# Kernel tuning notes

Hardware: AMD Instinct MI355X
Metric: run time of the kernel (lower is better)

The kernel has to match this reference:

```python
import jax, jax.numpy as jnp
import numpy as np

# Static configuration (mirrors init_kwargs)
F_REAL = 64
F_CAT = 32
OUT = 32
HID = [64, 64, 32]
IDX_REAL_MISS = np.arange(16)   # indices into the real-feature subset
IDX_CAT_MISS = np.arange(8)     # indices into the cat-feature subset
N_CAT_MISS = len(IDX_CAT_MISS)
B = 8192


def wn(v, g):
    """PyTorch weight_norm: w = g * v / ||v|| with norm over input dim (last axis).
    v: [F, out, in], g: [F, out] -> w: [F, out, in]"""
    return g[..., None] * v / jnp.linalg.norm(v, axis=-1, keepdims=True)


def setup_inputs() -> dict:
    key = jax.random.key(0)
    ks = jax.random.split(key, 16)
    s = 0.3
    values = jax.random.normal(ks[0], (B, 96), dtype=jnp.float32)
    miss = (jax.random.uniform(ks[1], (B, 96)) < 0.1).astype(jnp.float32)
    tabular = jnp.stack([values, miss], axis=1)  # [B, 2, 96]
    # Per-feature weight-normed MLP params, stacked over F_REAL features.
    inp = {
        "tabular": tabular,
        "v0": jax.random.normal(ks[2], (F_REAL, HID[0], 1)) * s,
        "g0": jnp.ones((F_REAL, HID[0])),
        "b0": jax.random.normal(ks[3], (F_REAL, HID[0])) * 0.01,
        "v1": jax.random.normal(ks[4], (F_REAL, HID[1], HID[0])) * s,
        "g1": jnp.ones((F_REAL, HID[1])),
        "b1": jax.random.normal(ks[5], (F_REAL, HID[1])) * 0.01,
        "v2": jax.random.normal(ks[6], (F_REAL, HID[2], HID[1])) * s,
        "g2": jnp.ones((F_REAL, HID[2])),
        "b2": jax.random.normal(ks[7], (F_REAL, HID[2])) * 0.01,
        "v3": jax.random.normal(ks[8], (F_REAL, OUT, HID[2])) * s,
        "g3": jnp.ones((F_REAL, OUT)),
        "cat_linear": jax.random.normal(ks[9], (F_CAT, OUT)) * s,
        "missing_emb": jax.random.normal(ks[10], (len(IDX_REAL_MISS) + N_CAT_MISS, OUT)) * s,
        "bias": jnp.zeros((1, OUT)),
    }
    return inp


def reference(tabular, v0, g0, b0, v1, g1, b1, v2, g2, b2, v3, g3,
              cat_linear, missing_emb, bias):
    # Eval mode: nn.Dropout / nn.Dropout1d are identity.
    values, is_missing = tabular[:, 0], tabular[:, 1]
    val_real, miss_real = values[:, :F_REAL], is_missing[:, :F_REAL]
    val_cat, miss_cat = values[:, F_REAL:F_REAL + F_CAT], is_missing[:, F_REAL:F_REAL + F_CAT]

    # Batched tiny MLPs over all real features at once.
    w0 = wn(v0, g0)[:, :, 0]                  # [F, H0] (scalar input)
    h = jax.nn.relu(val_real[:, :, None] * w0[None] + b0[None])        # [B,F,H0]
    h = jax.nn.relu(jnp.einsum('bfi,foi->bfo', h, wn(v1, g1)) + b1[None])  # [B,F,H1]
    h = jax.nn.relu(jnp.einsum('bfi,foi->bfo', h, wn(v2, g2)) + b2[None])  # [B,F,H2]
    feat_real = jnp.einsum('bfi,foi->bfo', h, wn(v3, g3))               # [B,F,OUT]

    feat_cat = cat_linear[None] * val_cat[:, :, None]                   # [B,Fc,OUT]

    feat_real = feat_real * (1.0 - miss_real[:, :, None])
    feat_cat = feat_cat * (1.0 - miss_cat[:, :, None])

    # Scatter-fill missing embeddings (add is exact since masked entries are zero)
    feat_real = feat_real.at[:, IDX_REAL_MISS, :].add(
        missing_emb[N_CAT_MISS:][None] * miss_real[:, IDX_REAL_MISS, None])
    feat_cat = feat_cat.at[:, IDX_CAT_MISS, :].add(
        missing_emb[:N_CAT_MISS][None] * miss_cat[:, IDX_CAT_MISS, None])

    features = jnp.concatenate([feat_real, feat_cat], axis=1)           # [B,96,OUT]
    logits = jnp.sum(features, axis=1) + bias                           # [B,OUT]
    return (logits, features)
```

## Files before the change

kernel.cpp:

```cpp
#include <hip/hip_runtime.h>
#include <math.h>

typedef _Float16 f16;
typedef _Float16 f16x8 __attribute__((ext_vector_type(8)));
typedef float f32x4 __attribute__((ext_vector_type(4)));

#define NB 8192
#define LOGN (NB * 32)

#define OFF_W0   0
#define OFF_SC1  16384
#define OFF_SC2  32768
#define OFF_SC3  40960
#define OFF_B1   49152
#define OFF_B2   573440
#define OFF_B3   835584
#define OFF_PART 966656
#define WS_NEED  (OFF_PART + 8ull * LOGN * 4ull)

__global__ __launch_bounds__(256)
void prep_norm(const float* __restrict__ v0, const float* __restrict__ g0,
               const float* __restrict__ v1, const float* __restrict__ g1,
               const float* __restrict__ v2, const float* __restrict__ g2,
               const float* __restrict__ v3, const float* __restrict__ g3,
               float* __restrict__ ws) {
    int t = blockIdx.x * blockDim.x + threadIdx.x;
    if (t < 4096) {
        float v = v0[t];
        ws[OFF_W0 / 4 + t] = g0[t] * (v >= 0.f ? 1.f : -1.f);
    } else if (t < 8192) {
        int r = t - 4096;
        const float* vp = v1 + (size_t)r * 64;
        float ss = 0.f;
        #pragma unroll
        for (int i = 0; i < 16; ++i) {
            float4 x = *(const float4*)(vp + i * 4);
            ss += x.x * x.x + x.y * x.y + x.z * x.z + x.w * x.w;
        }
        ws[OFF_SC1 / 4 + r] = g1[r] * __frsqrt_rn(ss);
    } else if (t < 10240) {
        int r = t - 8192;
        const float* vp = v2 + (size_t)r * 64;
        float ss = 0.f;
        #pragma unroll
        for (int i = 0; i < 16; ++i) {
            float4 x = *(const float4*)(vp + i * 4);
            ss += x.x * x.x + x.y * x.y + x.z * x.z + x.w * x.w;
        }
        ws[OFF_SC2 / 4 + r] = g2[r] * __frsqrt_rn(ss);
    } else if (t < 12288) {
        int r = t - 10240;
        const float* vp = v3 + (size_t)r * 32;
        float ss = 0.f;
        #pragma unroll
        for (int i = 0; i < 8; ++i) {
            float4 x = *(const float4*)(vp + i * 4);
            ss += x.x * x.x + x.y * x.y + x.z * x.z + x.w * x.w;
        }
        ws[OFF_SC3 / 4 + r] = g3[r] * __frsqrt_rn(ss);
    }
}

__global__ __launch_bounds__(256)
void prep_frag(const float* __restrict__ v1, const float* __restrict__ v2,
               const float* __restrict__ v3, const float* __restrict__ ws,
               f16* __restrict__ b1f, f16* __restrict__ b2f, f16* __restrict__ b3f) {
    int t = blockIdx.x * blockDim.x + threadIdx.x;
    if (t < 262144) {
        int i = t & 7, lane = (t >> 3) & 63, nt = (t >> 9) & 3, ks = (t >> 11) & 1, f = t >> 12;
        int k = ks * 32 + ((lane >> 4) << 3) + i;
        int n = nt * 16 + (lane & 15);
        int r = f * 64 + n;
        b1f[t] = (f16)(v1[(size_t)r * 64 + k] * ws[OFF_SC1 / 4 + r]);
    } else if (t < 393216) {
        int t2 = t - 262144;
        int i = t2 & 7, lane = (t2 >> 3) & 63, nt = (t2 >> 9) & 1, ks = (t2 >> 10) & 1, f = t2 >> 11;
        int k = ks * 32 + ((lane >> 4) << 3) + i;
        int n = nt * 16 + (lane & 15);
        int r = f * 32 + n;
        b2f[t2] = (f16)(v2[(size_t)r * 64 + k] * ws[OFF_SC2 / 4 + r]);
    } else {
        int t3 = t - 393216;
        int i = t3 & 7, lane = (t3 >> 3) & 63, nt = (t3 >> 9) & 1, f = t3 >> 10;
        int k = ((lane >> 4) << 3) + i;
        int n = nt * 16 + (lane & 15);
        int r = f * 32 + n;
        b3f[t3] = (f16)(v3[(size_t)r * 32 + k] * ws[OFF_SC3 / 4 + r]);
    }
}

__global__ __launch_bounds__(256, 2)
void nam_real_mfma(const float* __restrict__ tab, const float* __restrict__ w0,
                   const f16* __restrict__ b1f, const f16* __restrict__ b2f,
                   const f16* __restrict__ b3f,
                   const float* __restrict__ b0, const float* __restrict__ b1,
                   const float* __restrict__ b2, const float* __restrict__ memb,
                   float* __restrict__ feat, float* __restrict__ part) {
    __shared__ char lds[4][8192];
    __shared__ float tv[128][8];
    __shared__ float tm[128][8];
    const int wave = threadIdx.x >> 6, lane = threadIdx.x & 63;
    const int lq = lane >> 4, lr = lane & 15;
    const int rowbase = blockIdx.x * 128 + wave * 32;
    const int f0 = blockIdx.y * 8;
    char* h1b = lds[wave];
    char* h2b = lds[wave] + 4096;

    #pragma unroll
    for (int it = 0; it < 8; ++it) {
        int g = it * 256 + threadIdx.x;
        int row = g >> 4, w = g & 15;
        int col = (w < 8) ? (f0 + w) : (96 + f0 + (w - 8));
        float x = tab[(size_t)(blockIdx.x * 128 + row) * 192 + col];
        if (w < 8) tv[row][w] = x; else tm[row][w - 8] = x;
    }
    __syncthreads();

    float lacc[2][2][4];
    #pragma unroll
    for (int mt = 0; mt < 2; ++mt)
        #pragma unroll
        for (int nt = 0; nt < 2; ++nt)
            #pragma unroll
            for (int j = 0; j < 4; ++j) lacc[mt][nt][j] = 0.f;

    #pragma unroll 1
    for (int fi = 0; fi < 8; ++fi) {
        const int f = f0 + fi;

        f16x8 B1[2][4], B2[2][2], B3[2];
        {
            const f16* p1 = b1f + f * 4096 + lane * 8;
            #pragma unroll
            for (int ks = 0; ks < 2; ++ks)
                #pragma unroll
                for (int nt = 0; nt < 4; ++nt)
                    B1[ks][nt] = *(const f16x8*)(p1 + ks * 2048 + nt * 512);
            const f16* p2 = b2f + f * 2048 + lane * 8;
            #pragma unroll
            for (int ks = 0; ks < 2; ++ks)
                #pragma unroll
                for (int nt = 0; nt < 2; ++nt)
                    B2[ks][nt] = *(const f16x8*)(p2 + ks * 1024 + nt * 512);
            const f16* p3 = b3f + f * 1024 + lane * 8;
            #pragma unroll
            for (int nt = 0; nt < 2; ++nt)
                B3[nt] = *(const f16x8*)(p3 + nt * 512);
        }

        float b1v[4], b2v[2];
        #pragma unroll
        for (int nt = 0; nt < 4; ++nt) b1v[nt] = b1[f * 64 + nt * 16 + lr];
        #pragma unroll
        for (int nt = 0; nt < 2; ++nt) b2v[nt] = b2[f * 32 + nt * 16 + lr];
        float vmt[2];
        #pragma unroll
        for (int mt = 0; mt < 2; ++mt)
            vmt[mt] = tv[wave * 32 + mt * 16 + lr][fi];
        float ms[2][4];
        #pragma unroll
        for (int mt = 0; mt < 2; ++mt)
            #pragma unroll
            for (int j = 0; j < 4; ++j)
                ms[mt][j] = tm[wave * 32 + mt * 16 + lq * 4 + j][fi];

        f16x8 A0[2][2];
        #pragma unroll
        for (int ks = 0; ks < 2; ++ks) {
            float w0v[8], b0v[8];
            *(float4*)&w0v[0] = *(const float4*)(w0 + f * 64 + ks * 32 + lq * 8);
            *(float4*)&w0v[4] = *(const float4*)(w0 + f * 64 + ks * 32 + lq * 8 + 4);
            *(float4*)&b0v[0] = *(const float4*)(b0 + f * 64 + ks * 32 + lq * 8);
            *(float4*)&b0v[4] = *(const float4*)(b0 + f * 64 + ks * 32 + lq * 8 + 4);
            #pragma unroll
            for (int mt = 0; mt < 2; ++mt)
                #pragma unroll
                for (int i = 0; i < 8; ++i)
                    A0[mt][ks][i] = (f16)fmaxf(fmaf(vmt[mt], w0v[i], b0v[i]), 0.f);
        }

        f32x4 acc1[2][4];
        #pragma unroll
        for (int mt = 0; mt < 2; ++mt)
            #pragma unroll
            for (int nt = 0; nt < 4; ++nt) acc1[mt][nt] = (f32x4){0.f, 0.f, 0.f, 0.f};
        #pragma unroll
        for (int ks = 0; ks < 2; ++ks)
            #pragma unroll
            for (int nt = 0; nt < 4; ++nt)
                #pragma unroll
                for (int mt = 0; mt < 2; ++mt)
                    acc1[mt][nt] = __builtin_amdgcn_mfma_f32_16x16x32_f16(A0[mt][ks], B1[ks][nt], acc1[mt][nt], 0, 0, 0);
        #pragma unroll
        for (int mt = 0; mt < 2; ++mt)
            #pragma unroll
            for (int nt = 0; nt < 4; ++nt) {
                int n = nt * 16 + lr;
                int colb = ((n >> 3) << 4) + ((n & 7) << 1);
                #pragma unroll
                for (int j = 0; j < 4; ++j) {
                    int row = mt * 16 + lq * 4 + j;
                    int byte = ((row << 7) + colb) ^ ((row & 7) << 4);
                    *(f16*)(h1b + byte) = (f16)fmaxf(acc1[mt][nt][j] + b1v[nt], 0.f);
                }
            }

        f16x8 A1[2][2];
        #pragma unroll
        for (int mt = 0; mt < 2; ++mt)
            #pragma unroll
            for (int ks = 0; ks < 2; ++ks) {
                int row = mt * 16 + lr;
                int byte = ((row << 7) + ((ks * 4 + lq) << 4)) ^ ((row & 7) << 4);
                A1[mt][ks] = *(const f16x8*)(h1b + byte);
            }
        f32x4 acc2[2][2];
        #pragma unroll
        for (int mt = 0; mt < 2; ++mt)
            #pragma unroll
            for (int nt = 0; nt < 2; ++nt) acc2[mt][nt] = (f32x4){0.f, 0.f, 0.f, 0.f};
        #pragma unroll
        for (int ks = 0; ks < 2; ++ks)
            #pragma unroll
            for (int nt = 0; nt < 2; ++nt)
                #pragma unroll
                for (int mt = 0; mt < 2; ++mt)
                    acc2[mt][nt] = __builtin_amdgcn_mfma_f32_16x16x32_f16(A1[mt][ks], B2[ks][nt], acc2[mt][nt], 0, 0, 0);
        #pragma unroll
        for (int mt = 0; mt < 2; ++mt)
            #pragma unroll
            for (int nt = 0; nt < 2; ++nt) {
                int n = nt * 16 + lr;
                int colb = ((n >> 3) << 4) + ((n & 7) << 1);
                #pragma unroll
                for (int j = 0; j < 4; ++j) {
                    int row = mt * 16 + lq * 4 + j;
                    int byte = ((row << 7) + colb) ^ ((row & 7) << 4);
                    *(f16*)(h2b + byte) = (f16)fmaxf(acc2[mt][nt][j] + b2v[nt], 0.f);
                }
            }

        f16x8 A2[2];
        #pragma unroll
        for (int mt = 0; mt < 2; ++mt) {
            int row = mt * 16 + lr;
            int byte = ((row << 7) + (lq << 4)) ^ ((row & 7) << 4);
            A2[mt] = *(const f16x8*)(h2b + byte);
        }
        f32x4 acc3[2][2];
        #pragma unroll
        for (int mt = 0; mt < 2; ++mt)
            #pragma unroll
            for (int nt = 0; nt < 2; ++nt) acc3[mt][nt] = (f32x4){0.f, 0.f, 0.f, 0.f};
        #pragma unroll
        for (int nt = 0; nt < 2; ++nt)
            #pragma unroll
            for (int mt = 0; mt < 2; ++mt)
                acc3[mt][nt] = __builtin_amdgcn_mfma_f32_16x16x32_f16(A2[mt], B3[nt], acc3[mt][nt], 0, 0, 0);

        float e[2] = {0.f, 0.f};
        const bool hasemb = (f < 16);
        if (hasemb) {
            #pragma unroll
            for (int nt = 0; nt < 2; ++nt) e[nt] = memb[(8 + f) * 32 + nt * 16 + lr];
        }
        #pragma unroll
        for (int mt = 0; mt < 2; ++mt)
            #pragma unroll
            for (int nt = 0; nt < 2; ++nt) {
                int o = nt * 16 + lr;
                #pragma unroll
                for (int j = 0; j < 4; ++j) {
                    int row = rowbase + mt * 16 + lq * 4 + j;
                    float keep = 1.f - ms[mt][j];
                    float v = acc3[mt][nt][j] * keep;
                    if (hasemb) v = fmaf(e[nt], ms[mt][j], v);
                    feat[(size_t)row * 3072 + f * 32 + o] = v;
                    lacc[mt][nt][j] += v;
                }
            }
    }

    if (part) {
        float* pp = part + (size_t)blockIdx.y * LOGN;
        #pragma unroll
        for (int mt = 0; mt < 2; ++mt)
            #pragma unroll
            for (int nt = 0; nt < 2; ++nt)
                #pragma unroll
                for (int j = 0; j < 4; ++j) {
                    int row = rowbase + mt * 16 + lq * 4 + j;
                    pp[row * 32 + nt * 16 + lr] = lacc[mt][nt][j];
                }
    }
}

__global__ __launch_bounds__(256)
void nam_cat_reduce(const float* __restrict__ tab, const float* __restrict__ cat_linear,
                    const float* __restrict__ memb, const float* __restrict__ bias,
                    const float* __restrict__ part, float* __restrict__ feat,
                    float* __restrict__ logits) {
    int t = blockIdx.x * blockDim.x + threadIdx.x;
    int o = t & 31;
    int b = t >> 5;
    const float* tb = tab + (size_t)b * 192;
    float s = bias[o];
    if (part) {
        #pragma unroll
        for (int g = 0; g < 8; ++g) s += part[g * LOGN + t];
    }
    #pragma unroll
    for (int fc = 0; fc < 32; ++fc) {
        float val = tb[64 + fc];
        float miss = tb[160 + fc];
        float r = cat_linear[fc * 32 + o] * val * (1.f - miss);
        if (fc < 8) r = fmaf(memb[fc * 32 + o], miss, r);
        feat[(size_t)b * 3072 + (64 + fc) * 32 + o] = r;
        s += r;
    }
    if (part) logits[t] = s;
}

__global__ __launch_bounds__(256)
void nam_logits(const float* __restrict__ feat, const float* __restrict__ bias,
                float* __restrict__ logits) {
    int t = blockIdx.x * blockDim.x + threadIdx.x;
    int o = t & 31;
    int b = t >> 5;
    float s = bias[o];
    const float* fp = feat + (size_t)b * 3072 + o;
    #pragma unroll 8
    for (int f = 0; f < 96; ++f) s += fp[f * 32];
    logits[t] = s;
}

extern "C" void kernel_launch(void* const* d_in, const int* in_sizes, int n_in,
                              void* d_out, int out_size, void* d_ws, size_t ws_size,
                              hipStream_t stream) {
    const float* tab        = (const float*)d_in[0];
    const float* v0         = (const float*)d_in[1];
    const float* g0         = (const float*)d_in[2];
    const float* b0         = (const float*)d_in[3];
    const float* v1         = (const float*)d_in[4];
    const float* g1         = (const float*)d_in[5];
    const float* b1         = (const float*)d_in[6];
    const float* v2         = (const float*)d_in[7];
    const float* g2         = (const float*)d_in[8];
    const float* b2         = (const float*)d_in[9];
    const float* v3         = (const float*)d_in[10];
    const float* g3         = (const float*)d_in[11];
    const float* cat_linear = (const float*)d_in[12];
    const float* memb       = (const float*)d_in[13];
    const float* bias       = (const float*)d_in[14];

    float* out    = (float*)d_out;
    float* logits = out;
    float* feat   = out + LOGN;

    float* ws   = (float*)d_ws;
    float* w0   = (float*)((char*)d_ws + OFF_W0);
    f16*   b1f  = (f16*)((char*)d_ws + OFF_B1);
    f16*   b2f  = (f16*)((char*)d_ws + OFF_B2);
    f16*   b3f  = (f16*)((char*)d_ws + OFF_B3);
    float* part = (float*)((char*)d_ws + OFF_PART);
    const bool use_part = ws_size >= WS_NEED;
    float* partp = use_part ? part : nullptr;

    prep_norm<<<48, 256, 0, stream>>>(v0, g0, v1, g1, v2, g2, v3, g3, ws);
    prep_frag<<<1792, 256, 0, stream>>>(v1, v2, v3, ws, b1f, b2f, b3f);

    dim3 gr(64, 8);
    nam_real_mfma<<<gr, 256, 0, stream>>>(tab, w0, b1f, b2f, b3f, b0, b1, b2, memb, feat, partp);

    nam_cat_reduce<<<LOGN / 256, 256, 0, stream>>>(tab, cat_linear, memb, bias, partp, feat, logits);

    if (!use_part)
        nam_logits<<<LOGN / 256, 256, 0, stream>>>(feat, bias, logits);
}
```

Baseline: 48.00 us.

## Run cat kernel first and accumulate real-feature logits via atomics, transposed MFMA stores

The categorical kernel now runs before the MLP kernel, writing bias plus categorical contributions directly into logits. The real-feature kernel then atomically adds its per-block partial sums into logits, which removes the partial-sum workspace and the separate reduction pass. The layer-3 MFMA operands are swapped so each lane holds four contiguous output columns, allowing float4 feature stores instead of scalar stores. In exchange, the final logits depend on eight atomic adds per element, so summation order is no longer deterministic.

Result: slower. 72.84 us (+51.7%).

```diff
diff --git a/kernel.cpp b/kernel.cpp
--- a/kernel.cpp
+++ b/kernel.cpp
@@ -15,8 +15,6 @@
 #define OFF_B1   49152
 #define OFF_B2   573440
 #define OFF_B3   835584
-#define OFF_PART 966656
-#define WS_NEED  (OFF_PART + 8ull * LOGN * 4ull)
 
 __global__ __launch_bounds__(256)
 void prep_norm(const float* __restrict__ v0, const float* __restrict__ g0,
@@ -89,13 +87,49 @@
     }
 }
 
+__global__ __launch_bounds__(256)
+void nam_cat_base(const float* __restrict__ tab, const float* __restrict__ cat_linear,
+                  const float* __restrict__ memb, const float* __restrict__ bias,
+                  float* __restrict__ feat, float* __restrict__ logits) {
+    __shared__ float cl[1024];
+    __shared__ float mb[256];
+    __shared__ float bs[32];
+    for (int i = threadIdx.x; i < 1024; i += 256) cl[i] = cat_linear[i];
+    if (threadIdx.x < 256) mb[threadIdx.x] = memb[threadIdx.x];
+    if (threadIdx.x < 32) bs[threadIdx.x] = bias[threadIdx.x];
+    __syncthreads();
+
+    int t = blockIdx.x * blockDim.x + threadIdx.x;
+    int o = t & 31;
+    int b = t >> 5;
+    const float4* tb4 = (const float4*)(tab + (size_t)b * 192);
+    float* fb = feat + (size_t)b * 3072 + 64 * 32 + o;
+    float s = bs[o];
+    #pragma unroll
+    for (int q = 0; q < 8; ++q) {
+        float4 v4 = tb4[16 + q];
+        float4 m4 = tb4[40 + q];
+        float vv[4] = {v4.x, v4.y, v4.z, v4.w};
+        float mm[4] = {m4.x, m4.y, m4.z, m4.w};
+        #pragma unroll
+        for (int e = 0; e < 4; ++e) {
+            int fc = q * 4 + e;
+            float r = cl[fc * 32 + o] * vv[e] * (1.f - mm[e]);
+            if (fc < 8) r = fmaf(mb[fc * 32 + o], mm[e], r);
+            fb[fc * 32] = r;
+            s += r;
+        }
+    }
+    logits[t] = s;
+}
+
 __global__ __launch_bounds__(256, 2)
 void nam_real_mfma(const float* __restrict__ tab, const float* __restrict__ w0,
                    const f16* __restrict__ b1f, const f16* __restrict__ b2f,
                    const f16* __restrict__ b3f,
                    const float* __restrict__ b0, const float* __restrict__ b1,
                    const float* __restrict__ b2, const float* __restrict__ memb,
-                   float* __restrict__ feat, float* __restrict__ part) {
+                   float* __restrict__ feat, float* __restrict__ logits) {
     __shared__ char lds[4][8192];
     __shared__ float tv[128][8];
     __shared__ float tm[128][8];
@@ -153,16 +187,12 @@
         for (int nt = 0; nt < 4; ++nt) b1v[nt] = b1[f * 64 + nt * 16 + lr];
         #pragma unroll
         for (int nt = 0; nt < 2; ++nt) b2v[nt] = b2[f * 32 + nt * 16 + lr];
-        float vmt[2];
-        #pragma unroll
-        for (int mt = 0; mt < 2; ++mt)
+        float vmt[2], msr[2];
+        #pragma unroll
+        for (int mt = 0; mt < 2; ++mt) {
             vmt[mt] = tv[wave * 32 + mt * 16 + lr][fi];
-        float ms[2][4];
-        #pragma unroll
-        for (int mt = 0; mt < 2; ++mt)
-            #pragma unroll
-            for (int j = 0; j < 4; ++j)
-                ms[mt][j] = tm[wave * 32 + mt * 16 + lq * 4 + j][fi];
+            msr[mt] = tm[wave * 32 + mt * 16 + lr][fi];
+        }
 
         f16x8 A0[2][2];
         #pragma unroll
@@ -247,91 +277,62 @@
             int byte = ((row << 7) + (lq << 4)) ^ ((row & 7) << 4);
             A2[mt] = *(const f16x8*)(h2b + byte);
         }
-        f32x4 acc3[2][2];
-        #pragma unroll
-        for (int mt = 0; mt < 2; ++mt)
-            #pragma unroll
-            for (int nt = 0; nt < 2; ++nt) acc3[mt][nt] = (f32x4){0.f, 0.f, 0.f, 0.f};
+        f32x4 accT[2][2];
         #pragma unroll
         for (int nt = 0; nt < 2; ++nt)
             #pragma unroll
+            for (int mt = 0; mt < 2; ++mt) accT[nt][mt] = (f32x4){0.f, 0.f, 0.f, 0.f};
+        #pragma unroll
+        for (int nt = 0; nt < 2; ++nt)
+            #pragma unroll
             for (int mt = 0; mt < 2; ++mt)
-                acc3[mt][nt] = __builtin_amdgcn_mfma_f32_16x16x32_f16(A2[mt], B3[nt], acc3[mt][nt], 0, 0, 0);
-
-        float e[2] = {0.f, 0.f};
+                accT[nt][mt] = __builtin_amdgcn_mfma_f32_16x16x32_f16(B3[nt], A2[mt], accT[nt][mt], 0, 0, 0);
+
         const bool hasemb = (f < 16);
+        float4 e[2] = {{0,0,0,0},{0,0,0,0}};
         if (hasemb) {
             #pragma unroll
-            for (int nt = 0; nt < 2; ++nt) e[nt] = memb[(8 + f) * 32 + nt * 16 + lr];
-        }
-        #pragma unroll
-        for (int mt = 0; mt < 2; ++mt)
+            for (int nt = 0; nt < 2; ++nt)
+                e[nt] = *(const float4*)(memb + (8 + f) * 32 + nt * 16 + lq * 4);
+        }
+        #pragma unroll
+        for (int mt = 0; mt < 2; ++mt) {
+            const int row = rowbase + mt * 16 + lr;
+            const float m = msr[mt];
+            const float keep = 1.f - m;
+            float* dst = feat + (size_t)row * 3072 + f * 32 + lq * 4;
             #pragma unroll
             for (int nt = 0; nt < 2; ++nt) {
-                int o = nt * 16 + lr;
-                #pragma unroll
-                for (int j = 0; j < 4; ++j) {
-                    int row = rowbase + mt * 16 + lq * 4 + j;
-                    float keep = 1.f - ms[mt][j];
-                    float v = acc3[mt][nt][j] * keep;
-                    if (hasemb) v = fmaf(e[nt], ms[mt][j], v);
-                    feat[(size_t)row * 3072 + f * 32 + o] = v;
-                    lacc[mt][nt][j] += v;
+                float4 v;
+                v.x = accT[nt][mt][0] * keep;
+                v.y = accT[nt][mt][1] * keep;
+                v.z = accT[nt][mt][2] * keep;
+                v.w = accT[nt][mt][3] * keep;
+                if (hasemb) {
+                    v.x = fmaf(e[nt].x, m, v.x);
+                    v.y = fmaf(e[nt].y, m, v.y);
+                    v.z = fmaf(e[nt].z, m, v.z);
+                    v.w = fmaf(e[nt].w, m, v.w);
                 }
+                *(float4*)(dst + nt * 16) = v;
+                lacc[mt][nt][0] += v.x;
+                lacc[mt][nt][1] += v.y;
+                lacc[mt][nt][2] += v.z;
+                lacc[mt][nt][3] += v.w;
             }
-    }
-
-    if (part) {
-        float* pp = part + (size_t)blockIdx.y * LOGN;
-        #pragma unroll
-        for (int mt = 0; mt < 2; ++mt)
-            #pragma unroll
-            for (int nt = 0; nt < 2; ++nt)
-                #pragma unroll
-                for (int j = 0; j < 4; ++j) {
-                    int row = rowbase + mt * 16 + lq * 4 + j;
-                    pp[row * 32 + nt * 16 + lr] = lacc[mt][nt][j];
-                }
-    }
-}
-
-__global__ __launch_bounds__(256)
-void nam_cat_reduce(const float* __restrict__ tab, const float* __restrict__ cat_linear,
-                    const float* __restrict__ memb, const float* __restrict__ bias,
-                    const float* __restrict__ part, float* __restrict__ feat,
-                    float* __restrict__ logits) {
-    int t = blockIdx.x * blockDim.x + threadIdx.x;
-    int o = t & 31;
-    int b = t >> 5;
-    const float* tb = tab + (size_t)b * 192;
-    float s = bias[o];
-    if (part) {
-        #pragma unroll
-        for (int g = 0; g < 8; ++g) s += part[g * LOGN + t];
-    }
+        }
+    }
+
     #pragma unroll
-    for (int fc = 0; fc < 32; ++fc) {
-        float val = tb[64 + fc];
-        float miss = tb[160 + fc];
-        float r = cat_linear[fc * 32 + o] * val * (1.f - miss);
-        if (fc < 8) r = fmaf(memb[fc * 32 + o], miss, r);
-        feat[(size_t)b * 3072 + (64 + fc) * 32 + o] = r;
-        s += r;
-    }
-    if (part) logits[t] = s;
-}
-
-__global__ __launch_bounds__(256)
-void nam_logits(const float* __restrict__ feat, const float* __restrict__ bias,
-                float* __restrict__ logits) {
-    int t = blockIdx.x * blockDim.x + threadIdx.x;
-    int o = t & 31;
-    int b = t >> 5;
-    float s = bias[o];
-    const float* fp = feat + (size_t)b * 3072 + o;
-    #pragma unroll 8
-    for (int f = 0; f < 96; ++f) s += fp[f * 32];
-    logits[t] = s;
+    for (int mt = 0; mt < 2; ++mt) {
+        const int row = rowbase + mt * 16 + lr;
+        float* lp = logits + (size_t)row * 32 + lq * 4;
+        #pragma unroll
+        for (int nt = 0; nt < 2; ++nt)
+            #pragma unroll
+            for (int j = 0; j < 4; ++j)
+                atomicAdd(lp + nt * 16 + j, lacc[mt][nt][j]);
+    }
 }
 
 extern "C" void kernel_launch(void* const* d_in, const int* in_sizes, int n_in,
@@ -362,18 +363,12 @@
     f16*   b1f  = (f16*)((char*)d_ws + OFF_B1);
     f16*   b2f  = (f16*)((char*)d_ws + OFF_B2);
     f16*   b3f  = (f16*)((char*)d_ws + OFF_B3);
-    float* part = (float*)((char*)d_ws + OFF_PART);
-    const bool use_part = ws_size >= WS_NEED;
-    float* partp = use_part ? part : nullptr;
 
     prep_norm<<<48, 256, 0, stream>>>(v0, g0, v1, g1, v2, g2, v3, g3, ws);
     prep_frag<<<1792, 256, 0, stream>>>(v1, v2, v3, ws, b1f, b2f, b3f);
 
+    nam_cat_base<<<LOGN / 256, 256, 0, stream>>>(tab, cat_linear, memb, bias, feat, logits);
+
     dim3 gr(64, 8);
-    nam_real_mfma<<<gr, 256, 0, stream>>>(tab, w0, b1f, b2f, b3f, b0, b1, b2, memb, feat, partp);
-
-    nam_cat_reduce<<<LOGN / 256, 256, 0, stream>>>(tab, cat_linear, memb, bias, partp, feat, logits);
-
-    if (!use_part)
-        nam_logits<<<LOGN / 256, 256, 0, stream>>>(feat, bias, logits);
-}
+    nam_real_mfma<<<gr, 256, 0, stream>>>(tab, w0, b1f, b2f, b3f, b0, b1, b2, memb, feat, logits);
+}
```
